# Kernel tuning notes

Hardware: AMD Instinct MI355X
Metric: run time of the kernel (lower is better)

Reference implementation:

```python
import jax, jax.numpy as jnp
import numpy as np

D_MODEL = 1024
N_HEADS = 16
D_K = D_MODEL // N_HEADS


def setup_inputs() -> dict:
    key = jax.random.key(0)
    ks = jax.random.split(key, 12)
    B, S, D = 4, 2048, D_MODEL
    scale = 1.0 / np.sqrt(D)
    inp = {
        'query': jax.random.normal(ks[0], (B, S, D), jnp.float32),
        'key': jax.random.normal(ks[1], (B, S, D), jnp.float32),
        'value': jax.random.normal(ks[2], (B, S, D), jnp.float32),
        'Wq': jax.random.normal(ks[3], (D, D), jnp.float32) * scale,
        'bq': jax.random.normal(ks[4], (D,), jnp.float32) * 0.02,
        'Wk': jax.random.normal(ks[5], (D, D), jnp.float32) * scale,
        'bk': jax.random.normal(ks[6], (D,), jnp.float32) * 0.02,
        'Wv': jax.random.normal(ks[7], (D, D), jnp.float32) * scale,
        'bv': jax.random.normal(ks[8], (D,), jnp.float32) * 0.02,
        'Wo': jax.random.normal(ks[9], (D, D), jnp.float32) * scale,
        'bo': jax.random.normal(ks[10], (D,), jnp.float32) * 0.02,
    }
    return inp


def reference(query, key, value, Wq, bq, Wk, bk, Wv, bv, Wo, bo):
    B, S, D = query.shape
    # torch nn.Linear: y = x @ W^T + b
    def proj(x, W, b):
        y = jnp.einsum('bsd,ed->bse', x, W) + b
        # [B,S,D] -> [B,H,S,d_k]
        return y.reshape(B, S, N_HEADS, D_K).transpose(0, 2, 1, 3)

    q = proj(query, Wq, bq)
    k = proj(key, Wk, bk)
    v = proj(value, Wv, bv)

    scores = jnp.einsum('bhqd,bhkd->bhqk', q, k) / jnp.sqrt(jnp.float32(D_K))
    attn = jax.nn.softmax(scores, axis=-1)  # dropout = identity (eval mode)
    out = jnp.einsum('bhqk,bhkd->bhqd', attn, v)
    out = out.transpose(0, 2, 1, 3).reshape(B, S, D)
    return jnp.einsum('bsd,ed->bse', out, Wo) + bo
```

## Files before the change

kernel.cpp:

```cpp
#include <hip/hip_runtime.h>
#include <cstdint>
#include <cstddef>


#define BATCH   4
#define SEQ     2048
#define D_MODEL 1024
#define NHEADS  16
#define DK      64

typedef __attribute__((ext_vector_type(8))) __bf16 bf16x8_t;
typedef __attribute__((ext_vector_type(4))) float  f32x4;

__device__ inline unsigned short f2bf(float f) {
  union { float f; unsigned int i; } c; c.f = f;
  unsigned int i = c.i;
  i += 0x7FFFu + ((i >> 16) & 1u);
  return (unsigned short)(i >> 16);
}
__device__ inline unsigned int pack2(float lo, float hi) {
  return ((unsigned int)f2bf(lo)) | (((unsigned int)f2bf(hi)) << 16);
}
__device__ inline void cvt8(const float* __restrict__ src, unsigned short* __restrict__ dst) {
  const float4 a = *(const float4*)(src);
  const float4 b = *(const float4*)(src + 4);
  uint4 r;
  r.x = pack2(a.x, a.y); r.y = pack2(a.z, a.w);
  r.z = pack2(b.x, b.y); r.w = pack2(b.z, b.w);
  *(uint4*)dst = r;
}

typedef __attribute__((address_space(3))) unsigned int lds_u32_t;
typedef const __attribute__((address_space(1))) unsigned int glb_u32_t;
__device__ inline void gld16(const unsigned short* g, unsigned short* l) {
  __builtin_amdgcn_global_load_lds((glb_u32_t*)(uintptr_t)g,
                                   (lds_u32_t*)(unsigned int)(uintptr_t)l, 16, 0, 0);
}

__global__ __launch_bounds__(256) void cvt3_kernel(
    const float* __restrict__ a, const float* __restrict__ b, const float* __restrict__ c,
    unsigned short* __restrict__ oa, unsigned short* __restrict__ ob, unsigned short* __restrict__ oc)
{
  const float* s = (blockIdx.y == 0) ? a : (blockIdx.y == 1) ? b : c;
  unsigned short* d = (blockIdx.y == 0) ? oa : (blockIdx.y == 1) ? ob : oc;
  const size_t i = ((size_t)blockIdx.x * 256 + threadIdx.x) * 8;
  cvt8(s + i, d + i);
}
__global__ __launch_bounds__(256) void cvt4_kernel(
    const float* __restrict__ a, const float* __restrict__ b,
    const float* __restrict__ c, const float* __restrict__ dd,
    unsigned short* __restrict__ oa, unsigned short* __restrict__ ob,
    unsigned short* __restrict__ oc, unsigned short* __restrict__ od)
{
  const float* s = (blockIdx.y == 0) ? a : (blockIdx.y == 1) ? b : (blockIdx.y == 2) ? c : dd;
  unsigned short* d = (blockIdx.y == 0) ? oa : (blockIdx.y == 1) ? ob : (blockIdx.y == 2) ? oc : od;
  const size_t i = ((size_t)blockIdx.x * 256 + threadIdx.x) * 8;
  cvt8(s + i, d + i);
}

template <int OUT_QKV, int OUT_F32>
__global__ __launch_bounds__(256) void gemm_bt_kernel(
    const unsigned short* __restrict__ A,
    const unsigned short* __restrict__ W,
    const float* __restrict__ bias,
    void* __restrict__ Cv,
    int M, int N, int Kd, float oscale)
{
  __shared__ unsigned short a_lds[128 * 32];
  __shared__ unsigned short b_lds[128 * 32];

  const int tid  = threadIdx.x;
  const int lane = tid & 63;
  const int wv   = tid >> 6;
  const int l15  = lane & 15;
  const int quad = lane >> 4;
  const int m0 = blockIdx.x * 128;
  const int n0 = blockIdx.y * 128;
  const int wm = (wv & 1) * 64;
  const int wn = (wv >> 1) * 64;

  f32x4 acc[4][4];
  for (int i = 0; i < 4; ++i)
    for (int j = 0; j < 4; ++j)
      acc[i][j] = (f32x4){0.f, 0.f, 0.f, 0.f};

  const int srow = tid >> 2;
  const int sch  = (tid & 3) ^ (srow & 3);
  const unsigned short* Ap0 = A + (size_t)(m0 + srow) * Kd + sch * 8;
  const unsigned short* Ap1 = A + (size_t)(m0 + 64 + srow) * Kd + sch * 8;
  const unsigned short* Wp0 = W + (size_t)(n0 + srow) * Kd + sch * 8;
  const unsigned short* Wp1 = W + (size_t)(n0 + 64 + srow) * Kd + sch * 8;
  unsigned short* al0 = a_lds + wv * 512;
  unsigned short* al1 = a_lds + 2048 + wv * 512;
  unsigned short* bl0 = b_lds + wv * 512;
  unsigned short* bl1 = b_lds + 2048 + wv * 512;

  const int pq = (quad ^ (l15 & 3)) * 8;

  for (int k0 = 0; k0 < Kd; k0 += 32) {
    __syncthreads();
    gld16(Ap0 + k0, al0);
    gld16(Ap1 + k0, al1);
    gld16(Wp0 + k0, bl0);
    gld16(Wp1 + k0, bl1);
    __syncthreads();

    bf16x8_t af[4], bfr[4];
#pragma unroll
    for (int i = 0; i < 4; ++i)
      af[i] = *(const bf16x8_t*)&a_lds[(wm + i * 16 + l15) * 32 + pq];
#pragma unroll
    for (int j = 0; j < 4; ++j)
      bfr[j] = *(const bf16x8_t*)&b_lds[(wn + j * 16 + l15) * 32 + pq];

#pragma unroll
    for (int i = 0; i < 4; ++i)
#pragma unroll
      for (int j = 0; j < 4; ++j)
        acc[i][j] = __builtin_amdgcn_mfma_f32_16x16x32_bf16(af[i], bfr[j], acc[i][j], 0, 0, 0);
  }

  for (int j = 0; j < 4; ++j) {
    const int n = n0 + wn + j * 16 + l15;
    const float bv = bias[n];
    for (int i = 0; i < 4; ++i) {
      const int mbase = m0 + wm + i * 16 + quad * 4;
      for (int r = 0; r < 4; ++r) {
        const int m = mbase + r;
        const float v = (acc[i][j][r] + bv) * oscale;
        size_t off;
        if (OUT_QKV) {
          const int bb = m >> 11;
          const int ss = m & 2047;
          const int hh = n >> 6;
          const int dd = n & 63;
          off = (((size_t)bb * NHEADS + hh) * SEQ + ss) * DK + dd;
        } else {
          off = (size_t)m * N + n;
        }
        if (OUT_F32) ((float*)Cv)[off] = v;
        else         ((unsigned short*)Cv)[off] = f2bf(v);
      }
    }
  }
}

__global__ __launch_bounds__(256) void attn_kernel(
    const unsigned short* __restrict__ Q,
    const unsigned short* __restrict__ K,
    const unsigned short* __restrict__ V,
    unsigned short* __restrict__ Oattn)
{
  __shared__ unsigned short k_sw[64 * 64];
  __shared__ unsigned short vt_sw[64 * 64];
  __shared__ unsigned short pt_sw[4 * 16 * 64];

  const int tid  = threadIdx.x;
  const int lane = tid & 63;
  const int wv   = tid >> 6;
  const int l15  = lane & 15;
  const int quad = lane >> 4;
  const int q0   = blockIdx.x * 64;
  const int bh   = blockIdx.y;
  const size_t hoff = (size_t)bh * SEQ * DK;
  const unsigned short* Qh = Q + hoff;
  const unsigned short* Kh = K + hoff;
  const unsigned short* Vh = V + hoff;

  bf16x8_t qf0, qf1;
  {
    const unsigned short* qr = Qh + (size_t)(q0 + wv * 16 + l15) * DK;
    qf0 = *(const bf16x8_t*)(qr + quad * 8);
    qf1 = *(const bf16x8_t*)(qr + 32 + quad * 8);
  }

  f32x4 o[4];
#pragma unroll
  for (int t = 0; t < 4; ++t) o[t] = (f32x4){0.f, 0.f, 0.f, 0.f};
  float mval = -1e30f, lval = 0.f;

  const int kr = tid >> 3;
  const int c8 = tid & 7;
  const int swz_l15 = (l15 & 7) ^ (l15 >> 3);
  unsigned short* pt_base = pt_sw + wv * 1024;

  for (int kb = 0; kb < SEQ / 64; ++kb) {
    const int key0 = kb * 64;
    __syncthreads();

    {
      uint4 d0 = *(const uint4*)(Kh + (size_t)(key0 + kr) * DK + c8 * 8);
      uint4 d1 = *(const uint4*)(Kh + (size_t)(key0 + kr + 32) * DK + c8 * 8);
      const int r0 = kr, r1 = kr + 32;
      *(uint4*)&k_sw[r0 * 64 + ((c8 ^ ((r0 & 7) ^ (r0 >> 3))) << 3)] = d0;
      *(uint4*)&k_sw[r1 * 64 + ((c8 ^ ((r1 & 7) ^ (r1 >> 3))) << 3)] = d1;
    }
    {
      const unsigned short* vp = Vh + (size_t)(key0 + 2 * kr) * DK + c8 * 8;
      uint4 ra = *(const uint4*)vp;
      uint4 rb = *(const uint4*)(vp + DK);
      const unsigned int* pa = (const unsigned int*)&ra;
      const unsigned int* pb = (const unsigned int*)&rb;
      const int kchunk = kr >> 2;
      const int klo    = (2 * kr) & 7;
#pragma unroll
      for (int wd = 0; wd < 4; ++wd) {
        unsigned int av = pa[wd], bv = pb[wd];
        unsigned int colA = (bv << 16) | (av & 0xffffu);
        unsigned int colB = (bv & 0xffff0000u) | (av >> 16);
        const int d0 = c8 * 8 + wd * 2, d1 = d0 + 1;
        *(unsigned int*)&vt_sw[d0 * 64 + ((kchunk ^ ((d0 & 7) ^ (d0 >> 3))) << 3) + klo] = colA;
        *(unsigned int*)&vt_sw[d1 * 64 + ((kchunk ^ ((d1 & 7) ^ (d1 >> 3))) << 3) + klo] = colB;
      }
    }
    __syncthreads();

    f32x4 s[4];
#pragma unroll
    for (int t = 0; t < 4; ++t) {
      const int row = t * 16 + l15;
      const int sw  = (row & 7) ^ (row >> 3);
      bf16x8_t kf0 = *(const bf16x8_t*)&k_sw[row * 64 + ((quad ^ sw) << 3)];
      bf16x8_t kf1 = *(const bf16x8_t*)&k_sw[row * 64 + (((quad | 4) ^ sw) << 3)];
      f32x4 z = (f32x4){0.f, 0.f, 0.f, 0.f};
      z = __builtin_amdgcn_mfma_f32_16x16x32_bf16(kf0, qf0, z, 0, 0, 0);
      z = __builtin_amdgcn_mfma_f32_16x16x32_bf16(kf1, qf1, z, 0, 0, 0);
      s[t] = z;
    }

    float mx = s[0][0];
#pragma unroll
    for (int t = 0; t < 4; ++t)
#pragma unroll
      for (int r = 0; r < 4; ++r) mx = fmaxf(mx, s[t][r]);
    mx = fmaxf(mx, __shfl_xor(mx, 16));
    mx = fmaxf(mx, __shfl_xor(mx, 32));
    const float mnew  = fmaxf(mval, mx);
    const float alpha = __expf(mval - mnew);
    mval = mnew;
    float rs = 0.f;
    float p[4][4];
#pragma unroll
    for (int t = 0; t < 4; ++t)
#pragma unroll
      for (int r = 0; r < 4; ++r) { p[t][r] = __expf(s[t][r] - mnew); rs += p[t][r]; }
    rs += __shfl_xor(rs, 16);
    rs += __shfl_xor(rs, 32);
    lval = lval * alpha + rs;
#pragma unroll
    for (int t = 0; t < 4; ++t) o[t] *= alpha;

#pragma unroll
    for (int t = 0; t < 4; ++t) {
      const int chunk = 2 * t + (quad >> 1);
      unsigned short* dst = pt_base + l15 * 64 + ((chunk ^ swz_l15) << 3) + (quad & 1) * 4;
      *(uint2*)dst = make_uint2(pack2(p[t][0], p[t][1]), pack2(p[t][2], p[t][3]));
    }
    asm volatile("s_waitcnt lgkmcnt(0)" ::: "memory");

    bf16x8_t pf0 = *(const bf16x8_t*)(pt_base + l15 * 64 + ((quad ^ swz_l15) << 3));
    bf16x8_t pf1 = *(const bf16x8_t*)(pt_base + l15 * 64 + (((quad | 4) ^ swz_l15) << 3));

#pragma unroll
    for (int nt = 0; nt < 4; ++nt) {
      const int row = nt * 16 + l15;
      const int sw  = (row & 7) ^ (row >> 3);
      bf16x8_t vf0 = *(const bf16x8_t*)&vt_sw[row * 64 + ((quad ^ sw) << 3)];
      bf16x8_t vf1 = *(const bf16x8_t*)&vt_sw[row * 64 + (((quad | 4) ^ sw) << 3)];
      o[nt] = __builtin_amdgcn_mfma_f32_16x16x32_bf16(vf0, pf0, o[nt], 0, 0, 0);
      o[nt] = __builtin_amdgcn_mfma_f32_16x16x32_bf16(vf1, pf1, o[nt], 0, 0, 0);
    }
  }

  const int bb = bh >> 4, hh = bh & 15;
  const float inv = 1.0f / lval;
  unsigned short* orow = Oattn + (size_t)(bb * SEQ + q0 + wv * 16 + l15) * D_MODEL + hh * DK + quad * 4;
#pragma unroll
  for (int nt = 0; nt < 4; ++nt) {
    f32x4 v = o[nt];
    *(uint2*)(orow + nt * 16) = make_uint2(pack2(v[0] * inv, v[1] * inv),
                                           pack2(v[2] * inv, v[3] * inv));
  }
}

extern "C" void kernel_launch(void* const* d_in, const int* in_sizes, int n_in,
                              void* d_out, int out_size, void* d_ws, size_t ws_size,
                              hipStream_t stream) {
  const float* query = (const float*)d_in[0];
  const float* key   = (const float*)d_in[1];
  const float* value = (const float*)d_in[2];
  const float* Wq    = (const float*)d_in[3];
  const float* bq    = (const float*)d_in[4];
  const float* Wk    = (const float*)d_in[5];
  const float* bk    = (const float*)d_in[6];
  const float* Wv    = (const float*)d_in[7];
  const float* bv    = (const float*)d_in[8];
  const float* Wo    = (const float*)d_in[9];
  const float* bo    = (const float*)d_in[10];

  const size_t E  = (size_t)BATCH * SEQ * D_MODEL;
  const size_t WE = (size_t)D_MODEL * D_MODEL;
  unsigned short* ws  = (unsigned short*)d_ws;
  unsigned short* Qws = ws;
  unsigned short* Kws = ws + E;
  unsigned short* Vws = ws + 2 * E;
  unsigned short* qb  = ws + 3 * E;
  unsigned short* kb  = ws + 4 * E;
  unsigned short* vb  = ws + 5 * E;
  unsigned short* wqb = ws + 6 * E;
  unsigned short* wkb = wqb + WE;
  unsigned short* wvb = wqb + 2 * WE;
  unsigned short* wob = wqb + 3 * WE;
  unsigned short* Aws = qb;

  const int M = BATCH * SEQ;
  cvt3_kernel<<<dim3(E / 2048, 3), 256, 0, stream>>>(query, key, value, qb, kb, vb);
  cvt4_kernel<<<dim3(WE / 2048, 4), 256, 0, stream>>>(Wq, Wk, Wv, Wo, wqb, wkb, wvb, wob);

  dim3 gg(M / 128, D_MODEL / 128), blk(256);
  gemm_bt_kernel<1, 0><<<gg, blk, 0, stream>>>(qb, wqb, bq, Qws, M, D_MODEL, D_MODEL, 0.125f);
  gemm_bt_kernel<1, 0><<<gg, blk, 0, stream>>>(kb, wkb, bk, Kws, M, D_MODEL, D_MODEL, 1.0f);
  gemm_bt_kernel<1, 0><<<gg, blk, 0, stream>>>(vb, wvb, bv, Vws, M, D_MODEL, D_MODEL, 1.0f);
  attn_kernel<<<dim3(SEQ / 64, BATCH * NHEADS), blk, 0, stream>>>(Qws, Kws, Vws, Aws);
  gemm_bt_kernel<0, 1><<<gg, blk, 0, stream>>>(Aws, wob, bo, d_out, M, D_MODEL, D_MODEL, 1.0f);
}
```

Before: 431.6 us.

## Write V transposed from projection, async-load K/V tiles, merge QKV GEMMs, use exp2

The QKV projection becomes a single launch with a z-dimension selecting Q, K or V. V is written pre-transposed ([d,seq] per head) so the attention kernel can load K and V tiles straight into LDS with global_load_lds, dropping the register shuffle transpose. The Q scale folds in log2(e) so softmax can use the native exp2 instruction. The attention grid is also reordered to iterate heads in x, and bf16 conversion switches to the HIP intrinsic. The risks are scattered strided stores in the V epilogue and correctness of the swizzled direct LDS layout.

```diff
diff --git a/kernel.cpp b/kernel.cpp
--- a/kernel.cpp
+++ b/kernel.cpp
@@ -1,4 +1,5 @@
 #include <hip/hip_runtime.h>
+#include <hip/hip_bf16.h>
 #include <cstdint>
 #include <cstddef>
 
@@ -12,22 +13,25 @@
 typedef __attribute__((ext_vector_type(8))) __bf16 bf16x8_t;
 typedef __attribute__((ext_vector_type(4))) float  f32x4;
 
-__device__ inline unsigned short f2bf(float f) {
-  union { float f; unsigned int i; } c; c.f = f;
-  unsigned int i = c.i;
-  i += 0x7FFFu + ((i >> 16) & 1u);
-  return (unsigned short)(i >> 16);
-}
 __device__ inline unsigned int pack2(float lo, float hi) {
-  return ((unsigned int)f2bf(lo)) | (((unsigned int)f2bf(hi)) << 16);
-}
-__device__ inline void cvt8(const float* __restrict__ src, unsigned short* __restrict__ dst) {
-  const float4 a = *(const float4*)(src);
-  const float4 b = *(const float4*)(src + 4);
+  __hip_bfloat162 h = __float22bfloat162_rn(make_float2(lo, hi));
+  union { __hip_bfloat162 h; unsigned int u; } c; c.h = h; return c.u;
+}
+__device__ inline unsigned short f2bf(float f) { return (unsigned short)pack2(f, f); }
+
+#if __has_builtin(__builtin_amdgcn_exp2f)
+__device__ inline float fexp2(float x) { return __builtin_amdgcn_exp2f(x); }
+#else
+__device__ inline float fexp2(float x) { return __expf(x * 0.6931471805599453f); }
+#endif
+
+__device__ inline void cvt8(const float* __restrict__ s, unsigned short* __restrict__ d) {
+  const float4 a = *(const float4*)s;
+  const float4 b = *(const float4*)(s + 4);
   uint4 r;
   r.x = pack2(a.x, a.y); r.y = pack2(a.z, a.w);
   r.z = pack2(b.x, b.y); r.w = pack2(b.z, b.w);
-  *(uint4*)dst = r;
+  *(uint4*)d = r;
 }
 
 typedef __attribute__((address_space(3))) unsigned int lds_u32_t;
@@ -58,38 +62,25 @@
   cvt8(s + i, d + i);
 }
 
-template <int OUT_QKV, int OUT_F32>
-__global__ __launch_bounds__(256) void gemm_bt_kernel(
-    const unsigned short* __restrict__ A,
-    const unsigned short* __restrict__ W,
-    const float* __restrict__ bias,
-    void* __restrict__ Cv,
-    int M, int N, int Kd, float oscale)
-{
-  __shared__ unsigned short a_lds[128 * 32];
-  __shared__ unsigned short b_lds[128 * 32];
-
+__device__ inline void gemm_core(const unsigned short* __restrict__ A,
+                                 const unsigned short* __restrict__ W,
+                                 unsigned short* a_lds, unsigned short* b_lds,
+                                 int m0, int n0, f32x4 (&acc)[4][4])
+{
   const int tid  = threadIdx.x;
   const int lane = tid & 63;
   const int wv   = tid >> 6;
   const int l15  = lane & 15;
   const int quad = lane >> 4;
-  const int m0 = blockIdx.x * 128;
-  const int n0 = blockIdx.y * 128;
   const int wm = (wv & 1) * 64;
   const int wn = (wv >> 1) * 64;
 
-  f32x4 acc[4][4];
-  for (int i = 0; i < 4; ++i)
-    for (int j = 0; j < 4; ++j)
-      acc[i][j] = (f32x4){0.f, 0.f, 0.f, 0.f};
-
   const int srow = tid >> 2;
   const int sch  = (tid & 3) ^ (srow & 3);
-  const unsigned short* Ap0 = A + (size_t)(m0 + srow) * Kd + sch * 8;
-  const unsigned short* Ap1 = A + (size_t)(m0 + 64 + srow) * Kd + sch * 8;
-  const unsigned short* Wp0 = W + (size_t)(n0 + srow) * Kd + sch * 8;
-  const unsigned short* Wp1 = W + (size_t)(n0 + 64 + srow) * Kd + sch * 8;
+  const unsigned short* Ap0 = A + (size_t)(m0 + srow) * D_MODEL + sch * 8;
+  const unsigned short* Ap1 = Ap0 + (size_t)64 * D_MODEL;
+  const unsigned short* Wp0 = W + (size_t)(n0 + srow) * D_MODEL + sch * 8;
+  const unsigned short* Wp1 = Wp0 + (size_t)64 * D_MODEL;
   unsigned short* al0 = a_lds + wv * 512;
   unsigned short* al1 = a_lds + 2048 + wv * 512;
   unsigned short* bl0 = b_lds + wv * 512;
@@ -97,7 +88,7 @@
 
   const int pq = (quad ^ (l15 & 3)) * 8;
 
-  for (int k0 = 0; k0 < Kd; k0 += 32) {
+  for (int k0 = 0; k0 < D_MODEL; k0 += 32) {
     __syncthreads();
     gld16(Ap0 + k0, al0);
     gld16(Ap1 + k0, al1);
@@ -119,53 +110,131 @@
       for (int j = 0; j < 4; ++j)
         acc[i][j] = __builtin_amdgcn_mfma_f32_16x16x32_bf16(af[i], bfr[j], acc[i][j], 0, 0, 0);
   }
-
-  for (int j = 0; j < 4; ++j) {
-    const int n = n0 + wn + j * 16 + l15;
-    const float bv = bias[n];
-    for (int i = 0; i < 4; ++i) {
-      const int mbase = m0 + wm + i * 16 + quad * 4;
-      for (int r = 0; r < 4; ++r) {
-        const int m = mbase + r;
-        const float v = (acc[i][j][r] + bv) * oscale;
-        size_t off;
-        if (OUT_QKV) {
-          const int bb = m >> 11;
-          const int ss = m & 2047;
-          const int hh = n >> 6;
-          const int dd = n & 63;
-          off = (((size_t)bb * NHEADS + hh) * SEQ + ss) * DK + dd;
-        } else {
-          off = (size_t)m * N + n;
-        }
-        if (OUT_F32) ((float*)Cv)[off] = v;
-        else         ((unsigned short*)Cv)[off] = f2bf(v);
-      }
-    }
-  }
-}
-
-__global__ __launch_bounds__(256) void attn_kernel(
-    const unsigned short* __restrict__ Q,
-    const unsigned short* __restrict__ K,
-    const unsigned short* __restrict__ V,
-    unsigned short* __restrict__ Oattn)
-{
-  __shared__ unsigned short k_sw[64 * 64];
-  __shared__ unsigned short vt_sw[64 * 64];
-  __shared__ unsigned short pt_sw[4 * 16 * 64];
+}
+
+__global__ __launch_bounds__(256) void qkv_kernel(
+    const unsigned short* __restrict__ qb, const unsigned short* __restrict__ kb,
+    const unsigned short* __restrict__ vb,
+    const unsigned short* __restrict__ wq, const unsigned short* __restrict__ wk,
+    const unsigned short* __restrict__ wvp,
+    const float* __restrict__ bq, const float* __restrict__ bk, const float* __restrict__ bv,
+    unsigned short* __restrict__ Qws, unsigned short* __restrict__ Kws,
+    unsigned short* __restrict__ Vws)
+{
+  __shared__ unsigned short a_lds[128 * 32];
+  __shared__ unsigned short b_lds[128 * 32];
+
+  const int z = blockIdx.z;
+  const unsigned short* A = (z == 0) ? qb : (z == 1) ? kb : vb;
+  const unsigned short* W = (z == 0) ? wq : (z == 1) ? wk : wvp;
+  const float* bias       = (z == 0) ? bq : (z == 1) ? bk : bv;
+  unsigned short* C       = (z == 0) ? Qws : (z == 1) ? Kws : Vws;
+  const int m0 = blockIdx.x * 128;
+  const int n0 = blockIdx.y * 128;
+
+  f32x4 acc[4][4];
+#pragma unroll
+  for (int i = 0; i < 4; ++i)
+#pragma unroll
+    for (int j = 0; j < 4; ++j)
+      acc[i][j] = (f32x4){0.f, 0.f, 0.f, 0.f};
+
+  gemm_core(A, W, a_lds, b_lds, m0, n0, acc);
 
   const int tid  = threadIdx.x;
   const int lane = tid & 63;
   const int wv   = tid >> 6;
   const int l15  = lane & 15;
   const int quad = lane >> 4;
-  const int q0   = blockIdx.x * 64;
-  const int bh   = blockIdx.y;
+  const int wm = (wv & 1) * 64;
+  const int wn = (wv >> 1) * 64;
+  if (z == 2) {
+    for (int j = 0; j < 4; ++j) {
+      const int n = n0 + wn + j * 16 + l15;
+      const int hh = n >> 6, dd = n & 63;
+      const float bvl = bias[n];
+      for (int i = 0; i < 4; ++i) {
+        const int mbase = m0 + wm + i * 16 + quad * 4;
+        const int bb = mbase >> 11, ss = mbase & 2047;
+        uint2 w2 = make_uint2(pack2(acc[i][j][0] + bvl, acc[i][j][1] + bvl),
+                              pack2(acc[i][j][2] + bvl, acc[i][j][3] + bvl));
+        *(uint2*)(C + (((size_t)bb * NHEADS + hh) * DK + dd) * SEQ + ss) = w2;
+      }
+    }
+  } else {
+    const float oscale = (z == 0) ? 0.18033688011112042f : 1.0f;
+    for (int j = 0; j < 4; ++j) {
+      const int n = n0 + wn + j * 16 + l15;
+      const int hh = n >> 6, dd = n & 63;
+      const float bvl = bias[n];
+      for (int i = 0; i < 4; ++i) {
+        const int mbase = m0 + wm + i * 16 + quad * 4;
+        const int bb = mbase >> 11, ss = mbase & 2047;
+        unsigned short* dst = C + (((size_t)bb * NHEADS + hh) * SEQ + ss) * DK + dd;
+        for (int r = 0; r < 4; ++r)
+          dst[(size_t)r * DK] = f2bf((acc[i][j][r] + bvl) * oscale);
+      }
+    }
+  }
+}
+
+__global__ __launch_bounds__(256) void outproj_kernel(
+    const unsigned short* __restrict__ A, const unsigned short* __restrict__ W,
+    const float* __restrict__ bias, float* __restrict__ C)
+{
+  __shared__ unsigned short a_lds[128 * 32];
+  __shared__ unsigned short b_lds[128 * 32];
+  const int m0 = blockIdx.x * 128;
+  const int n0 = blockIdx.y * 128;
+
+  f32x4 acc[4][4];
+#pragma unroll
+  for (int i = 0; i < 4; ++i)
+#pragma unroll
+    for (int j = 0; j < 4; ++j)
+      acc[i][j] = (f32x4){0.f, 0.f, 0.f, 0.f};
+
+  gemm_core(A, W, a_lds, b_lds, m0, n0, acc);
+
+  const int tid  = threadIdx.x;
+  const int lane = tid & 63;
+  const int wv   = tid >> 6;
+  const int l15  = lane & 15;
+  const int quad = lane >> 4;
+  const int wm = (wv & 1) * 64;
+  const int wn = (wv >> 1) * 64;
+  for (int j = 0; j < 4; ++j) {
+    const int n = n0 + wn + j * 16 + l15;
+    const float bvl = bias[n];
+    for (int i = 0; i < 4; ++i) {
+      const int mbase = m0 + wm + i * 16 + quad * 4;
+      for (int r = 0; r < 4; ++r)
+        C[(size_t)(mbase + r) * D_MODEL + n] = acc[i][j][r] + bvl;
+    }
+  }
+}
+
+__global__ __launch_bounds__(256) void attn_kernel(
+    const unsigned short* __restrict__ Q,
+    const unsigned short* __restrict__ K,
+    const unsigned short* __restrict__ Vt,
+    unsigned short* __restrict__ Oattn)
+{
+  __shared__ unsigned short k_sw[64 * 64];
+  __shared__ unsigned short vt_sw[64 * 64];
+  __shared__ unsigned short pt_sw[4 * 16 * 64];
+
+  const int tid  = threadIdx.x;
+  const int lane = tid & 63;
+  const int wv   = tid >> 6;
+  const int l15  = lane & 15;
+  const int quad = lane >> 4;
+  const int bh   = blockIdx.x;
+  const int q0   = blockIdx.y * 64;
   const size_t hoff = (size_t)bh * SEQ * DK;
-  const unsigned short* Qh = Q + hoff;
-  const unsigned short* Kh = K + hoff;
-  const unsigned short* Vh = V + hoff;
+  const unsigned short* Qh  = Q  + hoff;
+  const unsigned short* Kh  = K  + hoff;
+  const unsigned short* Vth = Vt + hoff;
 
   bf16x8_t qf0, qf1;
   {
@@ -179,40 +248,31 @@
   for (int t = 0; t < 4; ++t) o[t] = (f32x4){0.f, 0.f, 0.f, 0.f};
   float mval = -1e30f, lval = 0.f;
 
-  const int kr = tid >> 3;
-  const int c8 = tid & 7;
+  const int sr = lane >> 3;
+  const int pc = lane & 7;
+  const int r0 = wv * 16 + sr;
+  const int r1 = r0 + 8;
+  const int sem0 = pc ^ (r0 & 7) ^ (r0 >> 3);
+  const int sem1 = pc ^ (r1 & 7) ^ (r1 >> 3);
+  const unsigned short* Ks0 = Kh  + (size_t)r0 * DK  + sem0 * 8;
+  const unsigned short* Ks1 = Kh  + (size_t)r1 * DK  + sem1 * 8;
+  const unsigned short* Vs0 = Vth + (size_t)r0 * SEQ + sem0 * 8;
+  const unsigned short* Vs1 = Vth + (size_t)r1 * SEQ + sem1 * 8;
+  unsigned short* kd0 = k_sw  + wv * 1024;
+  unsigned short* kd1 = k_sw  + wv * 1024 + 512;
+  unsigned short* vd0 = vt_sw + wv * 1024;
+  unsigned short* vd1 = vt_sw + wv * 1024 + 512;
+
   const int swz_l15 = (l15 & 7) ^ (l15 >> 3);
   unsigned short* pt_base = pt_sw + wv * 1024;
 
   for (int kb = 0; kb < SEQ / 64; ++kb) {
     const int key0 = kb * 64;
     __syncthreads();
-
-    {
-      uint4 d0 = *(const uint4*)(Kh + (size_t)(key0 + kr) * DK + c8 * 8);
-      uint4 d1 = *(const uint4*)(Kh + (size_t)(key0 + kr + 32) * DK + c8 * 8);
-      const int r0 = kr, r1 = kr + 32;
-      *(uint4*)&k_sw[r0 * 64 + ((c8 ^ ((r0 & 7) ^ (r0 >> 3))) << 3)] = d0;
-      *(uint4*)&k_sw[r1 * 64 + ((c8 ^ ((r1 & 7) ^ (r1 >> 3))) << 3)] = d1;
-    }
-    {
-      const unsigned short* vp = Vh + (size_t)(key0 + 2 * kr) * DK + c8 * 8;
-      uint4 ra = *(const uint4*)vp;
-      uint4 rb = *(const uint4*)(vp + DK);
-      const unsigned int* pa = (const unsigned int*)&ra;
-      const unsigned int* pb = (const unsigned int*)&rb;
-      const int kchunk = kr >> 2;
-      const int klo    = (2 * kr) & 7;
-#pragma unroll
-      for (int wd = 0; wd < 4; ++wd) {
-        unsigned int av = pa[wd], bv = pb[wd];
-        unsigned int colA = (bv << 16) | (av & 0xffffu);
-        unsigned int colB = (bv & 0xffff0000u) | (av >> 16);
-        const int d0 = c8 * 8 + wd * 2, d1 = d0 + 1;
-        *(unsigned int*)&vt_sw[d0 * 64 + ((kchunk ^ ((d0 & 7) ^ (d0 >> 3))) << 3) + klo] = colA;
-        *(unsigned int*)&vt_sw[d1 * 64 + ((kchunk ^ ((d1 & 7) ^ (d1 >> 3))) << 3) + klo] = colB;
-      }
-    }
+    gld16(Ks0 + (size_t)key0 * DK, kd0);
+    gld16(Ks1 + (size_t)key0 * DK, kd1);
+    gld16(Vs0 + key0, vd0);
+    gld16(Vs1 + key0, vd1);
     __syncthreads();
 
     f32x4 s[4];
@@ -236,14 +296,14 @@
     mx = fmaxf(mx, __shfl_xor(mx, 16));
     mx = fmaxf(mx, __shfl_xor(mx, 32));
     const float mnew  = fmaxf(mval, mx);
-    const float alpha = __expf(mval - mnew);
+    const float alpha = fexp2(mval - mnew);
     mval = mnew;
     float rs = 0.f;
     float p[4][4];
 #pragma unroll
     for (int t = 0; t < 4; ++t)
 #pragma unroll
-      for (int r = 0; r < 4; ++r) { p[t][r] = __expf(s[t][r] - mnew); rs += p[t][r]; }
+      for (int r = 0; r < 4; ++r) { p[t][r] = fexp2(s[t][r] - mnew); rs += p[t][r]; }
     rs += __shfl_xor(rs, 16);
     rs += __shfl_xor(rs, 32);
     lval = lval * alpha + rs;
@@ -313,14 +373,12 @@
   unsigned short* wob = wqb + 3 * WE;
   unsigned short* Aws = qb;
 
-  const int M = BATCH * SEQ;
   cvt3_kernel<<<dim3(E / 2048, 3), 256, 0, stream>>>(query, key, value, qb, kb, vb);
   cvt4_kernel<<<dim3(WE / 2048, 4), 256, 0, stream>>>(Wq, Wk, Wv, Wo, wqb, wkb, wvb, wob);
 
-  dim3 gg(M / 128, D_MODEL / 128), blk(256);
-  gemm_bt_kernel<1, 0><<<gg, blk, 0, stream>>>(qb, wqb, bq, Qws, M, D_MODEL, D_MODEL, 0.125f);
-  gemm_bt_kernel<1, 0><<<gg, blk, 0, stream>>>(kb, wkb, bk, Kws, M, D_MODEL, D_MODEL, 1.0f);
-  gemm_bt_kernel<1, 0><<<gg, blk, 0, stream>>>(vb, wvb, bv, Vws, M, D_MODEL, D_MODEL, 1.0f);
-  attn_kernel<<<dim3(SEQ / 64, BATCH * NHEADS), blk, 0, stream>>>(Qws, Kws, Vws, Aws);
-  gemm_bt_kernel<0, 1><<<gg, blk, 0, stream>>>(Aws, wob, bo, d_out, M, D_MODEL, D_MODEL, 1.0f);
-}
+  qkv_kernel<<<dim3(BATCH * SEQ / 128, D_MODEL / 128, 3), 256, 0, stream>>>(
+      qb, kb, vb, wqb, wkb, wvb, bq, bk, bv, Qws, Kws, Vws);
+  attn_kernel<<<dim3(BATCH * NHEADS, SEQ / 64), 256, 0, stream>>>(Qws, Kws, Vws, Aws);
+  outproj_kernel<<<dim3(BATCH * SEQ / 128, D_MODEL / 128), 256, 0, stream>>>(
+      Aws, wob, bo, (float*)d_out);
+}
```

Measured after the change: 403.0 us. 1.07x faster.
